# Kernel tuning notes

Hardware: AMD Instinct MI355X
Metric: run time of the kernel (lower is better)

The kernel has to match this reference:

```python
import jax, jax.numpy as jnp
import numpy as np

TAO = 3
M = 5
C_IN = 7
D_MODEL = 512
KERNELS = D_MODEL // C_IN          # 73
EXTRA = D_MODEL - C_IN * KERNELS   # 1


def _circular_conv1d(x_nct, w_oik, b_o):
    # Conv1d(kernel_size=3, padding=1, padding_mode='circular') == wrap-pad by 1 then VALID conv.
    xp = jnp.pad(x_nct, ((0, 0), (0, 0), (1, 1)), mode='wrap')
    out = jax.lax.conv_general_dilated(
        xp, w_oik, window_strides=(1,), padding='VALID',
        dimension_numbers=('NCH', 'OIH', 'NCH'))
    return out + b_o[None, :, None]


def setup_inputs() -> dict:
    key = jax.random.key(0)
    k1, k2, k3 = jax.random.split(key, 3)
    B, S = 32, 4096
    x = jax.random.normal(k1, (B, S, C_IN), dtype=jnp.float32)
    # kaiming_normal fan_in for Conv1d(in=m+1, k=3): std = sqrt(2/(1+0.01**2)) / sqrt((M+1)*3)
    std = float(np.sqrt(2.0 / (1.0 + 0.01 ** 2)) / np.sqrt((M + 1) * 3))
    w_conv = jax.random.normal(k2, (KERNELS, M + 1, 3), dtype=jnp.float32) * std
    b_conv = jnp.zeros((KERNELS,), dtype=jnp.float32)
    w_left = jax.random.normal(k3, (EXTRA, M + 1, 3), dtype=jnp.float32) * std
    b_left = jnp.zeros((EXTRA,), dtype=jnp.float32)
    return {"x": x, "w_conv": w_conv, "b_conv": b_conv, "w_left": w_left, "b_left": b_left}


def reference(x, w_conv, b_conv, w_left, b_left):
    B, S, C = x.shape
    L = S - M * TAO
    # time-delay gather: faithful vectors [x[t], x[t-tao], ..., x[t-m*tao]] per channel
    valid_t = jnp.arange(M * TAO, S)
    offs = jnp.arange(M + 1) * TAO
    idx = valid_t[:, None] - offs[None, :]            # [L, m+1]
    ext = x[:, idx, :]                                # [B, L, m+1, C]
    ext = jnp.transpose(ext, (0, 1, 3, 2))            # [B, L, C, m+1] (channel-major)
    emb = ext.reshape(B, L, C * (M + 1))
    emb = jnp.pad(emb, ((0, 0), (M * TAO, 0), (0, 0)))  # pad=True: left-pad time with zeros -> [B,S,C*(m+1)]
    # split into c_in chunks of (m+1) and run the SAME conv on each -> batch over (B*C)
    chunks = emb.reshape(B, S, C, M + 1).transpose(0, 2, 3, 1)  # [B, C, m+1, S]
    merged = chunks.reshape(B * C, M + 1, S)
    out = _circular_conv1d(merged, w_conv, b_conv)              # [B*C, K, S]
    out = out.reshape(B, C * KERNELS, S)                        # concat of per-chunk outputs
    # leftout conv on the LAST chunk only
    last = chunks[:, -1]                                        # [B, m+1, S]
    out_left = _circular_conv1d(last, w_left, b_left)           # [B, extra, S]
    out_full = jnp.concatenate([out, out_left], axis=1)         # [B, d_model, S]
    return jnp.transpose(out_full, (0, 2, 1))                   # [B, S, d_model]
```

## Files before the change

kernel.cpp:

```cpp
#include <hip/hip_runtime.h>

#define S      4096
#define CIN    7
#define DM     512
#define KERN   73
#define TT     256
#define TILES  (S / TT)
#define NSTAGE (TT + 17)
#define TROW   276
#define CHUNK  16
#define NCH    (TT / CHUNK)

__device__ __forceinline__ void do_chunk16(const float* __restrict__ xc,
                                           const float g[18], float bias,
                                           float* __restrict__ opc)
{
    float acc[CHUNK];
    #pragma unroll
    for (int i = 0; i < CHUNK; ++i) acc[i] = bias;

    #pragma unroll
    for (int q = 0; q < 9; ++q) {
        float4 v = *reinterpret_cast<const float4*>(xc + 4 * q);
        float va[4] = {v.x, v.y, v.z, v.w};
        #pragma unroll
        for (int e = 0; e < 4; ++e) {
            const int j = 4 * q + e;
            #pragma unroll
            for (int i = 0; i < CHUNK; ++i) {
                const int off = j - i;
                if (off >= 0 && off < 18)
                    acc[i] = fmaf(g[off], va[e], acc[i]);
            }
        }
        if (q == 4) {
            #pragma unroll
            for (int i = 0; i <= 2; ++i) opc[i * DM] = acc[i];
        }
        if (q == 5) {
            #pragma unroll
            for (int i = 3; i <= 6; ++i) opc[i * DM] = acc[i];
        }
        if (q == 6) {
            #pragma unroll
            for (int i = 7; i <= 10; ++i) opc[i * DM] = acc[i];
        }
        if (q == 7) {
            #pragma unroll
            for (int i = 11; i <= 14; ++i) opc[i * DM] = acc[i];
        }
        if (q == 8) {
            opc[15 * DM] = acc[15];
        }
    }
}

__global__ __launch_bounds__(512, 2)
void tokemb_kernel(const float* __restrict__ x,
                   const float* __restrict__ w_conv,
                   const float* __restrict__ b_conv,
                   const float* __restrict__ w_left,
                   const float* __restrict__ b_left,
                   float* __restrict__ out)
{
    __shared__ float xs[CIN * TROW];

    const int blk  = blockIdx.x;
    const int b    = blk / TILES;
    const int tile = blk & (TILES - 1);
    const int t0   = tile * TT;
    const int tid  = threadIdx.x;

    const float* xb = x + (long long)b * S * CIN;
    for (int e = tid; e < CIN * NSTAGE; e += 512) {
        int j = e / CIN, c = e - j * CIN;
        int tm = t0 - 16 + j;
        if (tm < 0) tm += S; else if (tm >= S) tm -= S;
        xs[c * TROW + j] = xb[tm * CIN + c];
    }

    const int d  = tid;
    const int oo = d % KERN;
    const float* wrow = (d < DM - 1) ? (w_conv + oo * 18) : w_left;
    const float bias  = (d < DM - 1) ? b_conv[oo] : b_left[0];
    const int cc = (d < DM - 1) ? (d / KERN) : (CIN - 1);
    float g[18];
    #pragma unroll
    for (int off = 0; off < 18; ++off)
        g[off] = wrow[(5 - off / 3) * 3 + (off % 3)];

    __syncthreads();

    const float* xrow = xs + cc * TROW;
    float* const op = out + ((long long)b * S + t0) * DM + d;

    const int wid = tid >> 6;
    const bool edgetile = (tile == 0) || (tile == TILES - 1);

    for (int cc_ = 0; cc_ < NCH; ++cc_) {
        const int ch  = ((cc_ + 2 * wid) & (NCH - 1));
        const int jb  = ch * CHUNK;
        const int tc  = t0 + jb;
        float* opc = op + jb * DM;

        if (!edgetile || !((tc < 16) || (tc + CHUNK >= S))) {
            do_chunk16(xrow + jb, g, bias, opc);
        } else {
            #pragma unroll
            for (int i = 0; i < CHUNK; ++i) {
                float p0 = 0.f, p1 = 0.f, p2 = 0.f;
                #pragma unroll
                for (int o = 0; o < 18; o += 3) {
                    p0 = fmaf(g[o],     xrow[jb + i + o],     p0);
                    p1 = fmaf(g[o + 1], xrow[jb + i + o + 1], p1);
                    p2 = fmaf(g[o + 2], xrow[jb + i + o + 2], p2);
                }
                const int t = tc + i;
                const float f0 = (t == 0 || t >= 16)     ? 1.f : 0.f;
                const float f1 = (t >= 15)               ? 1.f : 0.f;
                const float f2 = (t >= 14 && t != S - 1) ? 1.f : 0.f;
                opc[i * DM] = bias + f0 * p0 + f1 * p1 + f2 * p2;
            }
        }
    }
}

extern "C" void kernel_launch(void* const* d_in, const int* in_sizes, int n_in,
                              void* d_out, int out_size, void* d_ws, size_t ws_size,
                              hipStream_t stream) {
    const float* x      = (const float*)d_in[0];
    const float* w_conv = (const float*)d_in[1];
    const float* b_conv = (const float*)d_in[2];
    const float* w_left = (const float*)d_in[3];
    const float* b_left = (const float*)d_in[4];
    float* out = (float*)d_out;

    const int B = in_sizes[0] / (S * CIN);
    dim3 grid(B * TILES);
    tokemb_kernel<<<grid, 512, 0, stream>>>(x, w_conv, b_conv, w_left, b_left, out);
}
```

Baseline: 49.40 us.

## Widen per-thread time chunk to 32 and vectorize shared-memory staging

Each thread now computes 32 consecutive time steps per chunk instead of 16. This cuts the redundant shared-memory reads of the overlapping 17-element halo and the loop overhead, at the cost of more accumulator registers. The input tile is now loaded with float4 global reads where the range is in bounds, with a scalar fallback at the edges. The per-wavefront chunk rotation is adjusted for the new chunk count. The kernel is dominated by output writes, so these compute and load savings may matter little.

```diff
diff --git a/kernel.cpp b/kernel.cpp
--- a/kernel.cpp
+++ b/kernel.cpp
@@ -7,11 +7,11 @@
 #define TT     256
 #define TILES  (S / TT)
 #define NSTAGE (TT + 17)
-#define TROW   276
-#define CHUNK  16
+#define TROW   292
+#define CHUNK  32
 #define NCH    (TT / CHUNK)
 
-__device__ __forceinline__ void do_chunk16(const float* __restrict__ xc,
+__device__ __forceinline__ void do_chunk32(const float* __restrict__ xc,
                                            const float g[18], float bias,
                                            float* __restrict__ opc)
 {
@@ -20,7 +20,7 @@
     for (int i = 0; i < CHUNK; ++i) acc[i] = bias;
 
     #pragma unroll
-    for (int q = 0; q < 9; ++q) {
+    for (int q = 0; q < 13; ++q) {
         float4 v = *reinterpret_cast<const float4*>(xc + 4 * q);
         float va[4] = {v.x, v.y, v.z, v.w};
         #pragma unroll
@@ -33,24 +33,16 @@
                     acc[i] = fmaf(g[off], va[e], acc[i]);
             }
         }
-        if (q == 4) {
+        if (q >= 4 && q < 12) {
+            const int lo = (q == 4) ? 0 : (4 * q - 17);
+            const int hi = 4 * q - 14;
             #pragma unroll
-            for (int i = 0; i <= 2; ++i) opc[i * DM] = acc[i];
+            for (int i = 0; i < CHUNK; ++i)
+                if (i >= lo && i <= hi) opc[i * DM] = acc[i];
         }
-        if (q == 5) {
+        if (q == 12) {
             #pragma unroll
-            for (int i = 3; i <= 6; ++i) opc[i * DM] = acc[i];
-        }
-        if (q == 6) {
-            #pragma unroll
-            for (int i = 7; i <= 10; ++i) opc[i * DM] = acc[i];
-        }
-        if (q == 7) {
-            #pragma unroll
-            for (int i = 11; i <= 14; ++i) opc[i * DM] = acc[i];
-        }
-        if (q == 8) {
-            opc[15 * DM] = acc[15];
+            for (int i = 31; i <= 31; ++i) opc[i * DM] = acc[i];
         }
     }
 }
@@ -71,12 +63,34 @@
     const int t0   = tile * TT;
     const int tid  = threadIdx.x;
 
-    const float* xb = x + (long long)b * S * CIN;
-    for (int e = tid; e < CIN * NSTAGE; e += 512) {
-        int j = e / CIN, c = e - j * CIN;
-        int tm = t0 - 16 + j;
-        if (tm < 0) tm += S; else if (tm >= S) tm -= S;
-        xs[c * TROW + j] = xb[tm * CIN + c];
+    {
+        const float* xb = x + (long long)b * S * CIN;
+        const long long base = (long long)(t0 - 16) * CIN;
+        const int nfl = CIN * NSTAGE;
+        for (int e4 = 4 * tid; e4 < nfl; e4 += 4 * 512) {
+            long long src = base + e4;
+            if (src >= 0 && src + 3 < (long long)S * CIN) {
+                float4 v = *reinterpret_cast<const float4*>(xb + src);
+                float va[4] = {v.x, v.y, v.z, v.w};
+                #pragma unroll
+                for (int u = 0; u < 4; ++u) {
+                    int e = e4 + u;
+                    int j = e / CIN, c = e - j * CIN;
+                    xs[c * TROW + j] = va[u];
+                }
+            } else {
+                #pragma unroll
+                for (int u = 0; u < 4; ++u) {
+                    int e = e4 + u;
+                    if (e < nfl) {
+                        int j = e / CIN, c = e - j * CIN;
+                        int tm = t0 - 16 + j;
+                        if (tm < 0) tm += S; else if (tm >= S) tm -= S;
+                        xs[c * TROW + j] = xb[tm * CIN + c];
+                    }
+                }
+            }
+        }
     }
 
     const int d  = tid;
@@ -98,13 +112,13 @@
     const bool edgetile = (tile == 0) || (tile == TILES - 1);
 
     for (int cc_ = 0; cc_ < NCH; ++cc_) {
-        const int ch  = ((cc_ + 2 * wid) & (NCH - 1));
+        const int ch  = (cc_ + wid) & (NCH - 1);
         const int jb  = ch * CHUNK;
         const int tc  = t0 + jb;
         float* opc = op + jb * DM;
 
         if (!edgetile || !((tc < 16) || (tc + CHUNK >= S))) {
-            do_chunk16(xrow + jb, g, bias, opc);
+            do_chunk32(xrow + jb, g, bias, opc);
         } else {
             #pragma unroll
             for (int i = 0; i < CHUNK; ++i) {
```

Measured after the change: 48.59 us. Within noise of the previous version (-1.6%).
